# Optimization experiments

Measured on AMD Instinct MI355X. Metric: run time of the kernel, lower is better.

The kernel has to match this reference:

```python
import jax, jax.numpy as jnp
import numpy as np

N = 8192          # total samples = n_ways * num_instances
D = 512           # embedding dim
NUM_INSTANCES = 8 # shots per class
MARGIN = 0.3
W = 1.0
EPS = 1e-12


def setup_inputs() -> dict:
    key = jax.random.key(0)
    inputs = jax.random.normal(key, (N, D), dtype=jnp.float32)
    # targets[i] = class id; classes are contiguous blocks of NUM_INSTANCES
    targets = jnp.arange(N, dtype=jnp.int32) // NUM_INSTANCES
    return {"inputs": inputs, "targets": targets}


def _pairwise_euclid(a, b):
    # sqrt(clamp(||a||^2 + ||b||^2 - 2 a.b, eps)) -- same as torch addmm path
    sq_a = jnp.sum(a * a, axis=1)          # [na]
    sq_b = jnp.sum(b * b, axis=1)          # [nb]
    d2 = sq_a[:, None] + sq_b[None, :] - 2.0 * (a @ b.T)
    return jnp.sqrt(jnp.clip(d2, EPS, None))


def reference(inputs, targets):
    n = inputs.shape[0]
    n_ways = n // NUM_INSTANCES

    dist = _pairwise_euclid(inputs, inputs)              # [n, n]
    mask = targets[:, None] == targets[None, :]          # same-class mask

    # batch-hard mining: hardest positive (max same-class dist),
    # hardest negative (min different-class dist), fully vectorized
    dist_ap = jnp.max(jnp.where(mask, dist, -jnp.inf), axis=1)  # [n]
    dist_an = jnp.min(jnp.where(mask, jnp.inf, dist), axis=1)   # [n]

    # MarginRankingLoss with y=1: mean(relu(-(dist_an - dist_ap) + margin))
    loss = jnp.mean(jax.nn.relu(dist_ap - dist_an + MARGIN))

    dist_p = jnp.mean(dist_ap)
    dist_n = jnp.mean(dist_an)

    # prototype accuracy
    protos = inputs.reshape(n_ways, NUM_INSTANCES, -1).mean(axis=1)  # [n_ways, D]
    logits = _pairwise_euclid(inputs, protos)                        # [n, n_ways]
    estimate = jnp.argmin(logits, axis=1)
    labels = jnp.arange(n_ways, dtype=estimate.dtype).repeat(NUM_INSTANCES)
    acc = jnp.mean((estimate == labels).astype(jnp.float32))

    return (W * loss, acc, dist_p, dist_n)
```

## Files before the change

### kernel.cpp

```cpp
#include <hip/hip_runtime.h>
#include <hip/hip_bf16.h>
#include <stdint.h>

#define NTOT  8192
#define DIM   512
#define NI    8
#define NWAYS 1024
#define BM    256
#define BN    128
#define BK    128
#define NBUF  3
#define NSYM2 1056
#define NBLK2 1312
#define MARGINV 0.3f

typedef float f32x4 __attribute__((ext_vector_type(4)));

#define VMWAIT_BAR(N) \
  asm volatile("s_waitcnt vmcnt(" #N ")\n\ts_barrier" ::: "memory")

__device__ __forceinline__ unsigned f2o(float f) {
  unsigned u = __float_as_uint(f);
  return (u & 0x80000000u) ? ~u : (u | 0x80000000u);
}
__device__ __forceinline__ float o2f(unsigned u) {
  u = (u & 0x80000000u) ? (u & 0x7fffffffu) : ~u;
  return __uint_as_float(u);
}

__device__ __forceinline__ float wave_sum64(float v) {
#pragma unroll
  for (int s = 32; s; s >>= 1) v += __shfl_xor(v, s, 64);
  return v;
}

__device__ __forceinline__ void async_ld16(const void* g, void* l) {
  __builtin_amdgcn_global_load_lds(
      (__attribute__((address_space(1))) void*)(uintptr_t)g,
      (__attribute__((address_space(3))) void*)l, 16, 0, 0);
}

__global__ __launch_bounds__(256) void prep(
    const float* __restrict__ A, float* __restrict__ sq,
    float* __restrict__ psq, unsigned char* __restrict__ A8,
    unsigned char* __restrict__ P8,
    unsigned* __restrict__ an_u32, unsigned* __restrict__ ap_u32,
    unsigned long long* __restrict__ pr_key) {
  const int w = threadIdx.x >> 6;
  const int l = threadIdx.x & 63;
  const int b = blockIdx.x;
  if (b < NTOT / 4) {
    const int row = b * 4 + w;
    const float4* rp = (const float4*)(A + (size_t)row * DIM);
    unsigned* op = (unsigned*)(A8 + (size_t)row * DIM);
    float s = 0.f;
#pragma unroll
    for (int m = 0; m < 2; ++m) {
      const float4 v = rp[l + 64 * m];
      s = fmaf(v.x, v.x, fmaf(v.y, v.y, fmaf(v.z, v.z, fmaf(v.w, v.w, s))));
      int wd = 0;
      wd = __builtin_amdgcn_cvt_pk_fp8_f32(v.x, v.y, wd, false);
      wd = __builtin_amdgcn_cvt_pk_fp8_f32(v.z, v.w, wd, true);
      op[l + 64 * m] = (unsigned)wd;
    }
    s = wave_sum64(s);
    if (l == 0) {
      sq[row] = s;
      an_u32[row] = ~0u;
      ap_u32[row] = 0u;
      pr_key[row] = ~0ull;
    }
  } else {
    const int c = (b - NTOT / 4) * 4 + w;
    unsigned* op = (unsigned*)(P8 + (size_t)c * DIM);
    float s = 0.f;
#pragma unroll
    for (int m = 0; m < 2; ++m) {
      float4 p = {0.f, 0.f, 0.f, 0.f};
#pragma unroll
      for (int r = 0; r < NI; ++r) {
        const float4 v =
            ((const float4*)(A + (size_t)(c * NI + r) * DIM))[l + 64 * m];
        p.x += v.x; p.y += v.y; p.z += v.z; p.w += v.w;
      }
      p.x *= (1.f / NI); p.y *= (1.f / NI); p.z *= (1.f / NI); p.w *= (1.f / NI);
      s = fmaf(p.x, p.x, fmaf(p.y, p.y, fmaf(p.z, p.z, fmaf(p.w, p.w, s))));
      int wd = 0;
      wd = __builtin_amdgcn_cvt_pk_fp8_f32(p.x, p.y, wd, false);
      wd = __builtin_amdgcn_cvt_pk_fp8_f32(p.z, p.w, wd, true);
      op[l + 64 * m] = (unsigned)wd;
    }
    s = wave_sum64(s);
    if (l == 0) psq[c] = s;
  }
}

__global__ __launch_bounds__(512) void gemm_fused(
    const unsigned char* __restrict__ A, const unsigned char* __restrict__ P,
    const float* __restrict__ sq, const float* __restrict__ psq,
    unsigned* __restrict__ an_u32, unsigned* __restrict__ ap_u32,
    unsigned long long* __restrict__ pr_key) {
  __shared__ __align__(16) unsigned char As[NBUF][BM * BK];
  __shared__ __align__(16) unsigned char Bs[NBUF][BN * BK];
  __shared__ unsigned rmin[BM];
  __shared__ unsigned cmin[BN];
  __shared__ unsigned amax[BM];
  __shared__ unsigned long long rowkey[BM][2];

  const int braw = blockIdx.x;
  const int b = (braw & 7) * (NBLK2 / 8) + (braw >> 3);
  const bool isProto = b >= NSYM2;
  int I, J;
  const unsigned char* Bmat;
  const float* sqB;
  if (!isProto) {
    int rem = b, i = 0;
    while (rem >= 64 - 2 * i) { rem -= 64 - 2 * i; ++i; }
    I = i;
    J = 2 * i + rem;
    Bmat = A;
    sqB = sq;
  } else {
    const int p = b - NSYM2;
    I = p >> 3;
    J = p & 7;
    Bmat = P;
    sqB = psq;
  }
  const int rowBase = I * BM;
  const int colBase = J * BN;
  const int dh = J - 2 * I;
  const bool hasDiag = !isProto && (unsigned)dh <= 1u;

  const int t = threadIdx.x;
  const int lane = t & 63;
  const int wv = t >> 6;
  const int wr = wv >> 1;
  const int wc = wv & 1;
  const int quad = lane >> 4;
  const int lc = lane & 15;
  const bool diagHalf = !isProto && (2 * I + (wr >> 1)) == J;

  if (t < BM) { rmin[t] = ~0u; amax[t] = 0u; }
  if (t < BN) cmin[t] = ~0u;

  float sb[4];
#pragma unroll
  for (int y = 0; y < 4; ++y) sb[y] = sqB[colBase + wc * 64 + y * 16 + lc];
  float sa[4][4];
  if (!isProto) {
#pragma unroll
    for (int x = 0; x < 4; ++x)
#pragma unroll
      for (int r = 0; r < 4; ++r)
        sa[x][r] = sq[rowBase + wr * 64 + x * 16 + quad * 4 + r];
  }
  asm volatile("" ::: "memory");

  int koff[4];
#pragma unroll
  for (int c = 0; c < 4; ++c)
    koff[c] = (((c * 2 + (quad >> 1)) ^ (lc & 7)) * 16) + (quad & 1) * 8;

  int rowA[4], rowB[4];
#pragma unroll
  for (int x = 0; x < 4; ++x) {
    rowA[x] = (wr * 64 + x * 16 + lc) * BK;
    rowB[x] = (wc * 64 + x * 16 + lc) * BK;
  }

  const int l8 = lane >> 3;
  const int ul = ((lane & 7) ^ l8) * 16;
  const unsigned char* gA = A + (size_t)(rowBase + l8) * DIM + ul;
  const unsigned char* gB = Bmat + (size_t)(colBase + l8) * DIM + ul;
  const int ldsL = lane * 16;

#define STAGE(buf, tt)                                                        \
  do {                                                                        \
    _Pragma("unroll") for (int j = 0; j < 4; ++j) {                           \
      const int rr = wv * 4 + j;                                              \
      async_ld16(gA + (size_t)rr * 8 * DIM + (size_t)(tt) * BK,               \
                 &As[buf][rr * 1024 + ldsL]);                                 \
    }                                                                         \
    _Pragma("unroll") for (int j = 0; j < 2; ++j) {                           \
      const int rr = wv * 2 + j;                                              \
      async_ld16(gB + (size_t)rr * 8 * DIM + (size_t)(tt) * BK,               \
                 &Bs[buf][rr * 1024 + ldsL]);                                 \
    }                                                                         \
  } while (0)

  f32x4 acc[4][4] = {};

  STAGE(0, 0);
  STAGE(1, 1);

#pragma unroll
  for (int it = 0; it < 4; ++it) {
    if (it < 3) VMWAIT_BAR(6);
    else        VMWAIT_BAR(0);
    if (it < 2) STAGE((it + 2) % NBUF, it + 2);
    const unsigned char* Ac = &As[it % NBUF][0];
    const unsigned char* Bc = &Bs[it % NBUF][0];
#pragma unroll
    for (int c = 0; c < 4; ++c) {
      long af[4], bfr[4];
#pragma unroll
      for (int x = 0; x < 4; ++x) {
        af[x]  = *(const long*)(Ac + rowA[x] + koff[c]);
        bfr[x] = *(const long*)(Bc + rowB[x] + koff[c]);
      }
      __builtin_amdgcn_s_setprio(1);
#pragma unroll
      for (int x = 0; x < 4; ++x)
#pragma unroll
        for (int y = 0; y < 4; ++y)
          acc[x][y] = __builtin_amdgcn_mfma_f32_16x16x32_fp8_fp8(
              af[x], bfr[y], acc[x][y], 0, 0, 0);
      __builtin_amdgcn_s_setprio(0);
    }
  }
#undef STAGE

  const float INF = __int_as_float(0x7f800000);

  if (!isProto) {
#pragma unroll
    for (int x = 0; x < 4; ++x) {
#pragma unroll
      for (int r = 0; r < 4; ++r) {
        const int row = rowBase + wr * 64 + x * 16 + quad * 4 + r;
        float mv = INF, mx = -INF;
#pragma unroll
        for (int y = 0; y < 4; ++y) {
          const float v = fmaf(-2.f, acc[x][y][r], sb[y]);
          if (diagHalf) {
            const int col = colBase + wc * 64 + y * 16 + lc;
            const bool same = (row >> 3) == (col >> 3);
            mv = fminf(mv, same ? INF : v);
            mx = fmaxf(mx, same ? v : -INF);
          } else {
            mv = fminf(mv, v);
          }
        }
#pragma unroll
        for (int s = 1; s < 16; s <<= 1) {
          mv = fminf(mv, __shfl_xor(mv, s, 64));
          if (diagHalf) mx = fmaxf(mx, __shfl_xor(mx, s, 64));
        }
        if (lc == 0) {
          atomicMin(&rmin[row - rowBase], f2o(mv));
          if (diagHalf) atomicMax(&amax[row - rowBase], f2o(mx));
        }
      }
    }
    if (!diagHalf) {
#pragma unroll
      for (int y = 0; y < 4; ++y) {
        float cv = INF;
#pragma unroll
        for (int x = 0; x < 4; ++x)
#pragma unroll
          for (int r = 0; r < 4; ++r)
            cv = fminf(cv, fmaf(-2.f, acc[x][y][r], sa[x][r]));
        cv = fminf(cv, __shfl_xor(cv, 16, 64));
        cv = fminf(cv, __shfl_xor(cv, 32, 64));
        if (quad == 0) atomicMin(&cmin[wc * 64 + y * 16 + lc], f2o(cv));
      }
    }
  } else {
#pragma unroll
    for (int x = 0; x < 4; ++x) {
      unsigned long long kmin[4] = {~0ull, ~0ull, ~0ull, ~0ull};
#pragma unroll
      for (int y = 0; y < 4; ++y) {
        const int col = colBase + wc * 64 + y * 16 + lc;
#pragma unroll
        for (int r = 0; r < 4; ++r) {
          const float v = fmaf(-2.f, acc[x][y][r], sb[y]);
          const unsigned long long kn =
              ((unsigned long long)f2o(v) << 32) | (unsigned)col;
          if (kn < kmin[r]) kmin[r] = kn;
        }
      }
#pragma unroll
      for (int r = 0; r < 4; ++r) {
#pragma unroll
        for (int s = 1; s < 16; s <<= 1) {
          const unsigned long long o = __shfl_xor(kmin[r], s, 64);
          if (o < kmin[r]) kmin[r] = o;
        }
      }
      if (lc == 0) {
#pragma unroll
        for (int r = 0; r < 4; ++r)
          rowkey[wr * 64 + x * 16 + quad * 4 + r][wc] = kmin[r];
      }
    }
  }

  __syncthreads();
  if (isProto) {
    if (t < BM) {
      unsigned long long a = rowkey[t][0];
      const unsigned long long c = rowkey[t][1];
      if (c < a) a = c;
      atomicMin(pr_key + rowBase + t, a);
    }
  } else {
    if (t < BM) {
      atomicMin(an_u32 + rowBase + t, rmin[t]);
    } else if (t < BM + BN) {
      atomicMin(an_u32 + colBase + (t - BM), cmin[t - BM]);
    } else if (hasDiag && t < BM + BN + 128) {
      const int i = dh * 128 + (t - BM - BN);
      atomicMax(ap_u32 + rowBase + i, amax[i]);
    }
  }
}

__global__ void finalize_kernel(const float* __restrict__ sq,
                                const unsigned* __restrict__ an_u32,
                                const unsigned* __restrict__ ap_u32,
                                const unsigned long long* __restrict__ pr_key,
                                float* __restrict__ out) {
  const int tid = threadIdx.x;
  float loss = 0.f, sp = 0.f, sn = 0.f, acc = 0.f;
#pragma unroll
  for (int i = tid; i < NTOT; i += 1024) {
    const float s = sq[i];
    const float ap = sqrtf(fmaxf(s + o2f(ap_u32[i]), 1e-12f));
    const float an = sqrtf(fmaxf(s + o2f(an_u32[i]), 1e-12f));
    loss += fmaxf(ap - an + MARGINV, 0.f);
    sp += ap;
    sn += an;
    acc += ((unsigned)(pr_key[i] & 0xffffffffu) == (unsigned)(i >> 3)) ? 1.f : 0.f;
  }
  loss = wave_sum64(loss);
  sp = wave_sum64(sp);
  sn = wave_sum64(sn);
  acc = wave_sum64(acc);
  __shared__ float red[16][4];
  const int w = tid >> 6, l = tid & 63;
  if (l == 0) { red[w][0] = loss; red[w][1] = acc; red[w][2] = sp; red[w][3] = sn; }
  __syncthreads();
  if (tid == 0) {
    float L = 0, Ac = 0, Pm = 0, Nn = 0;
    for (int i = 0; i < 16; ++i) {
      L += red[i][0]; Ac += red[i][1]; Pm += red[i][2]; Nn += red[i][3];
    }
    out[0] = L / NTOT;
    out[1] = Ac / NTOT;
    out[2] = Pm / NTOT;
    out[3] = Nn / NTOT;
  }
}

extern "C" void kernel_launch(void* const* d_in, const int* in_sizes, int n_in,
                              void* d_out, int out_size, void* d_ws, size_t ws_size,
                              hipStream_t stream) {
  const float* inputs = (const float*)d_in[0];
  float* out = (float*)d_out;
  char* w = (char*)d_ws;
  float* sq  = (float*)(w);
  float* psq = (float*)(w + 32768);
  unsigned* an_u32 = (unsigned*)(w + 36864);
  unsigned* ap_u32 = (unsigned*)(w + 69632);
  unsigned long long* pr_key = (unsigned long long*)(w + 102400);
  unsigned char* A8 = (unsigned char*)(w + 167936);
  unsigned char* P8 = (unsigned char*)(w + 167936 + (size_t)NTOT * DIM);

  prep<<<NTOT / 4 + NWAYS / 4, 256, 0, stream>>>(inputs, sq, psq, A8, P8,
                                                 an_u32, ap_u32, pr_key);
  gemm_fused<<<NBLK2, 512, 0, stream>>>(A8, P8, sq, psq,
                                        an_u32, ap_u32, pr_key);
  finalize_kernel<<<1, 1024, 0, stream>>>(sq, an_u32, ap_u32, pr_key, out);
}
```

Baseline: 144.4 us.

## Make GEMM persistent with resident A row panel and streamed B tiles

Replaces the 1312-block grid with 256 persistent blocks, each handling a contiguous range of about five tile jobs ordered by row panel. The full 256x512 FP8 A panel stays in LDS and is reloaded only when the row panel changes, while B tiles stream through a triple buffer with BK=64. The LDS staging of per-row and per-column reductions is removed in favour of direct global atomics. This cuts repeated A loads and launch/tail overhead, at the cost of more global atomic traffic, larger LDS use (lower occupancy) and possible load imbalance across blocks.

Result: no change. 143.8 us (-0.4%).

```diff
diff --git a/kernel.cpp b/kernel.cpp
--- a/kernel.cpp
+++ b/kernel.cpp
@@ -8,16 +8,15 @@
 #define NWAYS 1024
 #define BM    256
 #define BN    128
-#define BK    128
-#define NBUF  3
-#define NSYM2 1056
-#define NBLK2 1312
+#define BK    64
+#define NJOBS 1312
 #define MARGINV 0.3f
 
 typedef float f32x4 __attribute__((ext_vector_type(4)));
 
 #define VMWAIT_BAR(N) \
   asm volatile("s_waitcnt vmcnt(" #N ")\n\ts_barrier" ::: "memory")
+#define SBAR() asm volatile("s_barrier" ::: "memory")
 
 __device__ __forceinline__ unsigned f2o(float f) {
   unsigned u = __float_as_uint(f);
@@ -100,37 +99,13 @@
     const float* __restrict__ sq, const float* __restrict__ psq,
     unsigned* __restrict__ an_u32, unsigned* __restrict__ ap_u32,
     unsigned long long* __restrict__ pr_key) {
-  __shared__ __align__(16) unsigned char As[NBUF][BM * BK];
-  __shared__ __align__(16) unsigned char Bs[NBUF][BN * BK];
-  __shared__ unsigned rmin[BM];
-  __shared__ unsigned cmin[BN];
-  __shared__ unsigned amax[BM];
-  __shared__ unsigned long long rowkey[BM][2];
+  __shared__ __align__(16) unsigned char As[BM * DIM];
+  __shared__ __align__(16) unsigned char Bs[3][BN * BK];
 
   const int braw = blockIdx.x;
-  const int b = (braw & 7) * (NBLK2 / 8) + (braw >> 3);
-  const bool isProto = b >= NSYM2;
-  int I, J;
-  const unsigned char* Bmat;
-  const float* sqB;
-  if (!isProto) {
-    int rem = b, i = 0;
-    while (rem >= 64 - 2 * i) { rem -= 64 - 2 * i; ++i; }
-    I = i;
-    J = 2 * i + rem;
-    Bmat = A;
-    sqB = sq;
-  } else {
-    const int p = b - NSYM2;
-    I = p >> 3;
-    J = p & 7;
-    Bmat = P;
-    sqB = psq;
-  }
-  const int rowBase = I * BM;
-  const int colBase = J * BN;
-  const int dh = J - 2 * I;
-  const bool hasDiag = !isProto && (unsigned)dh <= 1u;
+  const int b = (braw & 7) * 32 + (braw >> 3);
+  int job = (b * 41) >> 3;
+  const int jend = ((b + 1) * 41) >> 3;
 
   const int t = threadIdx.x;
   const int lane = t & 63;
@@ -139,181 +114,169 @@
   const int wc = wv & 1;
   const int quad = lane >> 4;
   const int lc = lane & 15;
-  const bool diagHalf = !isProto && (2 * I + (wr >> 1)) == J;
-
-  if (t < BM) { rmin[t] = ~0u; amax[t] = 0u; }
-  if (t < BN) cmin[t] = ~0u;
-
-  float sb[4];
-#pragma unroll
-  for (int y = 0; y < 4; ++y) sb[y] = sqB[colBase + wc * 64 + y * 16 + lc];
+
+  int koffA[16];
+#pragma unroll
+  for (int c = 0; c < 16; ++c)
+    koffA[c] = (((2 * c + (quad >> 1)) ^ (lc & 7)) << 4) + (quad & 1) * 8;
+  const int kf = (lc ^ (lc >> 2)) & 3;
+  int koffB[2];
+#pragma unroll
+  for (int cc = 0; cc < 2; ++cc)
+    koffB[cc] = (((cc * 2 + (quad >> 1)) ^ kf) << 4) + (quad & 1) * 8;
+  int rowA[4], rowB[4];
+#pragma unroll
+  for (int x = 0; x < 4; ++x) {
+    rowA[x] = (wr * 64 + x * 16 + lc) * DIM;
+    rowB[x] = (wc * 64 + x * 16 + lc) * BK;
+  }
+
+  const int bRow = wv * 16 + (lane >> 2);
+  const int bSu = ((lane & 3) ^ ((bRow ^ (bRow >> 2)) & 3)) << 4;
+  unsigned char* const bDst = &Bs[0][0] + wv * 1024 + lane * 16;
+  const int l32 = lane >> 5;
+
+  const float INF = __int_as_float(0x7f800000);
+
+  int curI = -1;
   float sa[4][4];
-  if (!isProto) {
-#pragma unroll
-    for (int x = 0; x < 4; ++x)
-#pragma unroll
-      for (int r = 0; r < 4; ++r)
-        sa[x][r] = sq[rowBase + wr * 64 + x * 16 + quad * 4 + r];
-  }
-  asm volatile("" ::: "memory");
-
-  int koff[4];
-#pragma unroll
-  for (int c = 0; c < 4; ++c)
-    koff[c] = (((c * 2 + (quad >> 1)) ^ (lc & 7)) * 16) + (quad & 1) * 8;
-
-  int rowA[4], rowB[4];
-#pragma unroll
-  for (int x = 0; x < 4; ++x) {
-    rowA[x] = (wr * 64 + x * 16 + lc) * BK;
-    rowB[x] = (wc * 64 + x * 16 + lc) * BK;
-  }
-
-  const int l8 = lane >> 3;
-  const int ul = ((lane & 7) ^ l8) * 16;
-  const unsigned char* gA = A + (size_t)(rowBase + l8) * DIM + ul;
-  const unsigned char* gB = Bmat + (size_t)(colBase + l8) * DIM + ul;
-  const int ldsL = lane * 16;
-
-#define STAGE(buf, tt)                                                        \
-  do {                                                                        \
-    _Pragma("unroll") for (int j = 0; j < 4; ++j) {                           \
-      const int rr = wv * 4 + j;                                              \
-      async_ld16(gA + (size_t)rr * 8 * DIM + (size_t)(tt) * BK,               \
-                 &As[buf][rr * 1024 + ldsL]);                                 \
-    }                                                                         \
-    _Pragma("unroll") for (int j = 0; j < 2; ++j) {                           \
-      const int rr = wv * 2 + j;                                              \
-      async_ld16(gB + (size_t)rr * 8 * DIM + (size_t)(tt) * BK,               \
-                 &Bs[buf][rr * 1024 + ldsL]);                                 \
-    }                                                                         \
-  } while (0)
-
-  f32x4 acc[4][4] = {};
-
-  STAGE(0, 0);
-  STAGE(1, 1);
-
-#pragma unroll
-  for (int it = 0; it < 4; ++it) {
-    if (it < 3) VMWAIT_BAR(6);
-    else        VMWAIT_BAR(0);
-    if (it < 2) STAGE((it + 2) % NBUF, it + 2);
-    const unsigned char* Ac = &As[it % NBUF][0];
-    const unsigned char* Bc = &Bs[it % NBUF][0];
-#pragma unroll
-    for (int c = 0; c < 4; ++c) {
-      long af[4], bfr[4];
+
+  for (; job < jend; ++job) {
+    int I = 0;
+    while ((I + 1) * (72 - I) <= job) ++I;
+    const int jl = job - I * (73 - I);
+    const bool sym = jl < 64 - 2 * I;
+    const int rowBase = I * BM;
+    const int colBase = (sym ? (2 * I + jl) : (jl - (64 - 2 * I))) * BN;
+    const unsigned char* Bsrc = sym ? A : P;
+    const float* sqB = sym ? sq : psq;
+    const bool diagHalf = sym && (jl == (wr >> 1));
+
+    if (I != curI) {
+      curI = I;
+      const unsigned char* gAp = A + (size_t)rowBase * DIM;
+#pragma unroll
+      for (int j = 0; j < 16; ++j) {
+        const int row = wv * 32 + 2 * j + l32;
+        async_ld16(gAp + (size_t)row * DIM + (((lane & 31) ^ (row & 7)) << 4),
+                   &As[(wv * 32 + 2 * j) * DIM + lane * 16]);
+      }
+#pragma unroll
+      for (int x = 0; x < 4; ++x)
+#pragma unroll
+        for (int r = 0; r < 4; ++r)
+          sa[x][r] = sq[rowBase + wr * 64 + x * 16 + quad * 4 + r];
+    }
+
+    float sb[4];
+#pragma unroll
+    for (int y = 0; y < 4; ++y) sb[y] = sqB[colBase + wc * 64 + y * 16 + lc];
+
+    const unsigned char* gB = Bsrc + (size_t)(colBase + bRow) * DIM + bSu;
+    async_ld16(gB + 0 * BK, bDst + 0 * 8192);
+    async_ld16(gB + 1 * BK, bDst + 1 * 8192);
+
+    f32x4 acc[4][4] = {};
+#pragma unroll
+    for (int kt = 0; kt < 8; ++kt) {
+      if (kt < 7) VMWAIT_BAR(1);
+      else        VMWAIT_BAR(0);
+      if (kt < 6)
+        async_ld16(gB + (size_t)(kt + 2) * BK, bDst + ((kt + 2) % 3) * 8192);
+      const unsigned char* Bc = &Bs[kt % 3][0];
+#pragma unroll
+      for (int cc = 0; cc < 2; ++cc) {
+        long af[4], bf[4];
+#pragma unroll
+        for (int x = 0; x < 4; ++x) {
+          af[x] = *(const long*)(As + rowA[x] + koffA[kt * 2 + cc]);
+          bf[x] = *(const long*)(Bc + rowB[x] + koffB[cc]);
+        }
+        __builtin_amdgcn_s_setprio(1);
+#pragma unroll
+        for (int x = 0; x < 4; ++x)
+#pragma unroll
+          for (int y = 0; y < 4; ++y)
+            acc[x][y] = __builtin_amdgcn_mfma_f32_16x16x32_fp8_fp8(
+                af[x], bf[y], acc[x][y], 0, 0, 0);
+        __builtin_amdgcn_s_setprio(0);
+      }
+    }
+    SBAR();
+
+    if (sym) {
 #pragma unroll
       for (int x = 0; x < 4; ++x) {
-        af[x]  = *(const long*)(Ac + rowA[x] + koff[c]);
-        bfr[x] = *(const long*)(Bc + rowB[x] + koff[c]);
-      }
-      __builtin_amdgcn_s_setprio(1);
-#pragma unroll
-      for (int x = 0; x < 4; ++x)
-#pragma unroll
-        for (int y = 0; y < 4; ++y)
-          acc[x][y] = __builtin_amdgcn_mfma_f32_16x16x32_fp8_fp8(
-              af[x], bfr[y], acc[x][y], 0, 0, 0);
-      __builtin_amdgcn_s_setprio(0);
-    }
-  }
-#undef STAGE
-
-  const float INF = __int_as_float(0x7f800000);
-
-  if (!isProto) {
-#pragma unroll
-    for (int x = 0; x < 4; ++x) {
-#pragma unroll
-      for (int r = 0; r < 4; ++r) {
-        const int row = rowBase + wr * 64 + x * 16 + quad * 4 + r;
-        float mv = INF, mx = -INF;
+#pragma unroll
+        for (int r = 0; r < 4; ++r) {
+          const int row = rowBase + wr * 64 + x * 16 + quad * 4 + r;
+          float mv = INF, mx = -INF;
+#pragma unroll
+          for (int y = 0; y < 4; ++y) {
+            const float v = fmaf(-2.f, acc[x][y][r], sb[y]);
+            if (diagHalf) {
+              const int col = colBase + wc * 64 + y * 16 + lc;
+              const bool same = (row >> 3) == (col >> 3);
+              mv = fminf(mv, same ? INF : v);
+              mx = fmaxf(mx, same ? v : -INF);
+            } else {
+              mv = fminf(mv, v);
+            }
+          }
+#pragma unroll
+          for (int s = 1; s < 16; s <<= 1) {
+            mv = fminf(mv, __shfl_xor(mv, s, 64));
+            if (diagHalf) mx = fmaxf(mx, __shfl_xor(mx, s, 64));
+          }
+          if (lc == 0) {
+            atomicMin(&an_u32[row], f2o(mv));
+            if (diagHalf) atomicMax(&ap_u32[row], f2o(mx));
+          }
+        }
+      }
+      if (!diagHalf) {
 #pragma unroll
         for (int y = 0; y < 4; ++y) {
-          const float v = fmaf(-2.f, acc[x][y][r], sb[y]);
-          if (diagHalf) {
-            const int col = colBase + wc * 64 + y * 16 + lc;
-            const bool same = (row >> 3) == (col >> 3);
-            mv = fminf(mv, same ? INF : v);
-            mx = fmaxf(mx, same ? v : -INF);
-          } else {
-            mv = fminf(mv, v);
-          }
-        }
-#pragma unroll
-        for (int s = 1; s < 16; s <<= 1) {
-          mv = fminf(mv, __shfl_xor(mv, s, 64));
-          if (diagHalf) mx = fmaxf(mx, __shfl_xor(mx, s, 64));
-        }
-        if (lc == 0) {
-          atomicMin(&rmin[row - rowBase], f2o(mv));
-          if (diagHalf) atomicMax(&amax[row - rowBase], f2o(mx));
-        }
-      }
-    }
-    if (!diagHalf) {
-#pragma unroll
-      for (int y = 0; y < 4; ++y) {
-        float cv = INF;
-#pragma unroll
-        for (int x = 0; x < 4; ++x)
-#pragma unroll
-          for (int r = 0; r < 4; ++r)
-            cv = fminf(cv, fmaf(-2.f, acc[x][y][r], sa[x][r]));
-        cv = fminf(cv, __shfl_xor(cv, 16, 64));
-        cv = fminf(cv, __shfl_xor(cv, 32, 64));
-        if (quad == 0) atomicMin(&cmin[wc * 64 + y * 16 + lc], f2o(cv));
-      }
-    }
-  } else {
-#pragma unroll
-    for (int x = 0; x < 4; ++x) {
-      unsigned long long kmin[4] = {~0ull, ~0ull, ~0ull, ~0ull};
-#pragma unroll
-      for (int y = 0; y < 4; ++y) {
-        const int col = colBase + wc * 64 + y * 16 + lc;
+          float cv = INF;
+#pragma unroll
+          for (int x = 0; x < 4; ++x)
+#pragma unroll
+            for (int r = 0; r < 4; ++r)
+              cv = fminf(cv, fmaf(-2.f, acc[x][y][r], sa[x][r]));
+          cv = fminf(cv, __shfl_xor(cv, 16, 64));
+          cv = fminf(cv, __shfl_xor(cv, 32, 64));
+          if (quad == 0)
+            atomicMin(&an_u32[colBase + wc * 64 + y * 16 + lc], f2o(cv));
+        }
+      }
+    } else {
+#pragma unroll
+      for (int x = 0; x < 4; ++x) {
+        unsigned long long kmin[4] = {~0ull, ~0ull, ~0ull, ~0ull};
+#pragma unroll
+        for (int y = 0; y < 4; ++y) {
+          const int col = colBase + wc * 64 + y * 16 + lc;
+#pragma unroll
+          for (int r = 0; r < 4; ++r) {
+            const float v = fmaf(-2.f, acc[x][y][r], sb[y]);
+            const unsigned long long kn =
+                ((unsigned long long)f2o(v) << 32) | (unsigned)col;
+            if (kn < kmin[r]) kmin[r] = kn;
+          }
+        }
 #pragma unroll
         for (int r = 0; r < 4; ++r) {
-          const float v = fmaf(-2.f, acc[x][y][r], sb[y]);
-          const unsigned long long kn =
-              ((unsigned long long)f2o(v) << 32) | (unsigned)col;
-          if (kn < kmin[r]) kmin[r] = kn;
-        }
-      }
-#pragma unroll
-      for (int r = 0; r < 4; ++r) {
-#pragma unroll
-        for (int s = 1; s < 16; s <<= 1) {
-          const unsigned long long o = __shfl_xor(kmin[r], s, 64);
-          if (o < kmin[r]) kmin[r] = o;
-        }
-      }
-      if (lc == 0) {
-#pragma unroll
-        for (int r = 0; r < 4; ++r)
-          rowkey[wr * 64 + x * 16 + quad * 4 + r][wc] = kmin[r];
-      }
-    }
-  }
-
-  __syncthreads();
-  if (isProto) {
-    if (t < BM) {
-      unsigned long long a = rowkey[t][0];
-      const unsigned long long c = rowkey[t][1];
-      if (c < a) a = c;
-      atomicMin(pr_key + rowBase + t, a);
-    }
-  } else {
-    if (t < BM) {
-      atomicMin(an_u32 + rowBase + t, rmin[t]);
-    } else if (t < BM + BN) {
-      atomicMin(an_u32 + colBase + (t - BM), cmin[t - BM]);
-    } else if (hasDiag && t < BM + BN + 128) {
-      const int i = dh * 128 + (t - BM - BN);
-      atomicMax(ap_u32 + rowBase + i, amax[i]);
+#pragma unroll
+          for (int s = 1; s < 16; s <<= 1) {
+            const unsigned long long o = __shfl_xor(kmin[r], s, 64);
+            if (o < kmin[r]) kmin[r] = o;
+          }
+          if (lc == 0) {
+            const int row = rowBase + wr * 64 + x * 16 + quad * 4 + r;
+            atomicMin(&pr_key[row], kmin[r]);
+          }
+        }
+      }
     }
   }
 }
@@ -371,7 +334,7 @@
 
   prep<<<NTOT / 4 + NWAYS / 4, 256, 0, stream>>>(inputs, sq, psq, A8, P8,
                                                  an_u32, ap_u32, pr_key);
-  gemm_fused<<<NBLK2, 512, 0, stream>>>(A8, P8, sq, psq,
-                                        an_u32, ap_u32, pr_key);
+  gemm_fused<<<256, 512, 0, stream>>>(A8, P8, sq, psq,
+                                      an_u32, ap_u32, pr_key);
   finalize_kernel<<<1, 1024, 0, stream>>>(sq, an_u32, ap_u32, pr_key, out);
 }
```
